# Kernel optimization log

Measured on AMD Instinct MI355X. Metric: run time of the kernel, lower is better.

Reference implementation:

```python
import jax, jax.numpy as jnp
import numpy as np

POS_MARGIN = 0.1
NEG_MARGIN = 1.4
LOG_SCALE = 24.0
MAX_POINTS = 256

N_FULL = 50000
M_C = 2048
N_C = 2048
D_FEAT = 256
K_CORR = 4096
N_BACK = 30000


def setup_inputs() -> dict:
    key = jax.random.key(0)
    ks = jax.random.split(key, 12)
    ref_feats = jax.random.normal(ks[4], (M_C, D_FEAT), jnp.float32)
    src_feats = jax.random.normal(ks[5], (N_C, D_FEAT), jnp.float32)
    # features are assumed L2-normalized (pairwise_distance(..., normalized=True))
    ref_feats = ref_feats / jnp.linalg.norm(ref_feats, axis=-1, keepdims=True)
    src_feats = src_feats / jnp.linalg.norm(src_feats, axis=-1, keepdims=True)
    return {
        "ref_points": jax.random.normal(ks[0], (N_FULL, 3), jnp.float32),
        "src_points": jax.random.normal(ks[1], (N_FULL, 3), jnp.float32),
        "ref_points_c": jax.random.normal(ks[2], (M_C, 3), jnp.float32),
        "src_points_c": jax.random.normal(ks[3], (N_C, 3), jnp.float32),
        "ref_feats_c": ref_feats,
        "src_feats_c": src_feats,
        "gt_node_corr_indices": jax.random.randint(ks[6], (K_CORR, 2), 0, M_C, dtype=jnp.int64) if jax.config.jax_enable_x64 else jax.random.randint(ks[6], (K_CORR, 2), 0, M_C, dtype=jnp.int32),
        "gt_node_corr_overlaps": jax.random.uniform(ks[7], (K_CORR,), jnp.float32),
        "corr_sp_mask": jax.random.uniform(ks[8], (M_C + N_C,), jnp.float32),
        "ref_back_indices": jax.random.randint(ks[9], (N_BACK,), 0, N_FULL, dtype=jnp.int32),
        "src_back_indices": jax.random.randint(ks[10], (N_BACK,), 0, N_FULL, dtype=jnp.int32),
    }


def _nn_indices(full_points, corr_points):
    # argmin over squared euclidean distance == argmin over cdist(p=2)
    d = (jnp.sum(corr_points ** 2, axis=1)[:, None]
         + jnp.sum(full_points ** 2, axis=1)[None, :]
         - 2.0 * corr_points @ full_points.T)  # [k, N]
    return jnp.argmin(d, axis=1)


def _forward(ref_points, src_points, ref_points_c, src_points_c,
             ref_feats_c, src_feats_c, gt_node_corr_overlaps, corr_sp_mask,
             gt_node_corr_indices, ref_back_indices, src_back_indices):
    m = ref_feats_c.shape[0]
    n = src_feats_c.shape[0]

    idx_ref = _nn_indices(ref_points, ref_points_c)  # [m]
    idx_src = _nn_indices(src_points, src_points_c)  # [n]

    # mask_ref[i] True iff idx_ref[i] appears in ref_back_indices (set intersection semantics)
    mask_ref = jnp.any(idx_ref[:, None] == ref_back_indices[None, :], axis=1)
    mask_src = jnp.any(idx_src[:, None] == src_back_indices[None, :], axis=1)

    xi = gt_node_corr_indices[:, 0]
    yi = gt_node_corr_indices[:, 1]
    corr_gt = jnp.zeros((m, n), dtype=bool).at[xi, yi].set(True)
    corr_overlap = jnp.zeros((m, n), jnp.float32).at[xi, yi].set(gt_node_corr_overlaps)

    corr_gt = corr_gt & (mask_ref[:, None] & mask_src[None, :])
    gt_mask = jnp.concatenate([mask_ref, mask_src]).astype(jnp.float32)  # [m+n]

    # cap number of positives at MAX_POINTS by overlap score
    count = jnp.sum(corr_gt)
    score = jnp.where(corr_gt, corr_overlap, -1.0).reshape(-1)
    topv, topi = jax.lax.top_k(score, MAX_POINTS)
    capped = jnp.zeros((m * n,), dtype=bool).at[topi].set(topv > -0.5).reshape(m, n)
    corr_gt = jnp.where(count > MAX_POINTS, capped, corr_gt)

    var_mask = 1.0 - corr_sp_mask  # [m+n]

    # NLLLaplace
    feat_sq = jnp.maximum(2.0 - 2.0 * (ref_feats_c @ src_feats_c.T), 0.0)
    feat_dists = jnp.sqrt(feat_sq)  # [m, n]
    laplace_mask = var_mask[:m][:, None] * var_mask[m:m + n][None, :]
    feat_dists = jnp.exp(0.5 * laplace_mask) * feat_dists

    not_pos = (~corr_gt).astype(jnp.float32)
    not_neg = corr_gt.astype(jnp.float32)
    pos_w = jax.lax.stop_gradient(
        jnp.maximum(feat_dists - 100000.0 * not_pos - POS_MARGIN, 0.0))
    neg_w = jax.lax.stop_gradient(
        jnp.maximum(NEG_MARGIN - (feat_dists + 100000.0 * not_neg), 0.0))

    lp = LOG_SCALE * (feat_dists - POS_MARGIN) * pos_w
    ln = LOG_SCALE * (NEG_MARGIN - feat_dists) * neg_w
    loss_row = jax.nn.softplus(jax.nn.logsumexp(lp, axis=-1) + jax.nn.logsumexp(ln, axis=-1)) / LOG_SCALE
    loss_col = jax.nn.softplus(jax.nn.logsumexp(lp, axis=-2) + jax.nn.logsumexp(ln, axis=-2)) / LOG_SCALE
    loss1 = (jnp.mean(loss_row) + jnp.mean(loss_col)) / 2.0
    loss2 = jnp.mean(jnp.abs(var_mask - gt_mask))
    loss = loss1 + loss2
    return loss, loss1, loss2


def reference(ref_points, src_points, ref_points_c, src_points_c,
              ref_feats_c, src_feats_c, gt_node_corr_indices,
              gt_node_corr_overlaps, corr_sp_mask,
              ref_back_indices, src_back_indices):
    return _forward(ref_points, src_points, ref_points_c, src_points_c,
                    ref_feats_c, src_feats_c, gt_node_corr_overlaps, corr_sp_mask,
                    gt_node_corr_indices, ref_back_indices, src_back_indices)
```

## Files before the change

### kernel.cpp

```cpp
#include <hip/hip_runtime.h>
#include <math.h>

using u8  = unsigned char;
using u32 = unsigned int;
using u64 = unsigned long long;

typedef short short8 __attribute__((ext_vector_type(8)));
typedef float f32x4  __attribute__((ext_vector_type(4)));
typedef float f32x2  __attribute__((ext_vector_type(2)));

#define MC 2048
#define NC 2048
#define DF 256
#define NFULL 50000
#define NBACK 30000
#define KCORR 4096
#define MAXPTS 256
#define NN_CHUNK 196
#define BM_WORDS_I 1568

constexpr size_t OFF_ROWP = 0;
constexpr size_t OFF_COLP = (size_t)2 * 1024 * 1024;
constexpr size_t OFF_GTB  = (size_t)3 * 1024 * 1024;
constexpr size_t OFF_NN   = OFF_GTB + (size_t)512 * 1024;
constexpr size_t OFF_CAND = OFF_NN + 4096 * 8;
constexpr size_t OFF_ACC  = OFF_CAND + 4096 * 8;
constexpr size_t OFF_CNT  = OFF_ACC + 256;
constexpr size_t OFF_BM   = OFF_CNT + 256;
constexpr size_t OFF_KMAX = (size_t)4 * 1024 * 1024;


__device__ __forceinline__ u32 mask_of(const u64* nn, const u32* bm, int idx, int side) {
    u32 j = (u32)(nn[idx] & 0xFFFFFFFFull);
    return (bm[side * BM_WORDS_I + (j >> 5)] >> (j & 31)) & 1u;
}

__device__ __forceinline__ void circle_terms(float d, bool g, float& lp, float& ln) {
    if (g) { float a = d - 0.1f; lp = a > 0.f ? 24.f*a*a : 0.f; ln = 0.f; }
    else   { float b = 1.4f - d; ln = b > 0.f ? 24.f*b*b : 0.f; lp = 0.f; }
}

__device__ __forceinline__ float softplus_(float x) {
    return fmaxf(x, 0.f) + log1pf(expf(-fabsf(x)));
}

__device__ __forceinline__ void lse_merge(float& M, float& S, float M2, float S2) {
    float nm = fmaxf(M, M2);
    S = S * expf(M - nm) + S2 * expf(M2 - nm);
    M = nm;
}

__device__ __forceinline__ void block_barrier(u32* counter, u32 target, u32* s_tic) {
    __threadfence();
    __syncthreads();
    if (threadIdx.x == 0) {
        *s_tic = atomicAdd(counter, 1u);
        while (__hip_atomic_load(counter, __ATOMIC_ACQUIRE, __HIP_MEMORY_SCOPE_AGENT) < target) {}
    }
    __syncthreads();
}

__global__ __launch_bounds__(256) void k_init(uint4* __restrict__ gtb4, u64* __restrict__ nn,
                                              float* __restrict__ acc, u32* __restrict__ cnt,
                                              u32* __restrict__ bm, uint4* __restrict__ kmax4) {
    int e = blockIdx.x * 256 + threadIdx.x;
    #pragma unroll
    for (int u = 0; u < 4; ++u)
        kmax4[e + u * 262144] = make_uint4(0u, 0u, 0u, 0u);
    if (e < 32768) gtb4[e] = make_uint4(0u, 0u, 0u, 0u);
    if (e < 4096) nn[e] = ~0ull;
    if (e < 2 * BM_WORDS_I) bm[e] = 0u;
    if (e < 8) acc[e] = 0.f;
    if (e < 8) cnt[e] = 0u;
}

__global__ __launch_bounds__(256) void k_nn(
        const float* __restrict__ fr, const float* __restrict__ fs,
        const float* __restrict__ cr, const float* __restrict__ cs,
        const int* __restrict__ rbi, const int* __restrict__ sbi,
        u32* __restrict__ bm, u64* __restrict__ nn) {
    const int side = blockIdx.y;
    const float* full = side ? fs : fr;
    const float* corr = side ? cs : cr;
    const int ib = blockIdx.x & 3, ch = blockIdx.x >> 2;
    const int t = threadIdx.x;

    int gb = side * 1024 + blockIdx.x;
    if (gb < 235) {
        int e = gb * 256 + t;
        if (e < 2 * NBACK) {
            int s2 = e < NBACK ? 0 : 1;
            int v = s2 ? sbi[e - NBACK] : rbi[e];
            atomicOr(&bm[s2 * BM_WORDS_I + (v >> 5)], 1u << (v & 31));
        }
    }

    __shared__ float4 sx4[49], sy4[49], sz4[49], sw4[49];
    const int j0 = ch * NN_CHUNK;
    if (t < 49) {
        int b4 = j0 + t * 4;
        float xx[4], yy[4], zz[4], ww[4];
        #pragma unroll
        for (int u = 0; u < 4; ++u) {
            int j = b4 + u;
            if (j < NFULL) {
                float x = full[j*3], y = full[j*3+1], z = full[j*3+2];
                xx[u] = x; yy[u] = y; zz[u] = z;
                ww[u] = fmaf(x, x, fmaf(y, y, z*z));
            } else {
                xx[u] = 0.f; yy[u] = 0.f; zz[u] = 0.f; ww[u] = 3.0e38f;
            }
        }
        sx4[t] = make_float4(xx[0], xx[1], xx[2], xx[3]);
        sy4[t] = make_float4(yy[0], yy[1], yy[2], yy[3]);
        sz4[t] = make_float4(zz[0], zz[1], zz[2], zz[3]);
        sw4[t] = make_float4(ww[0], ww[1], ww[2], ww[3]);
    }

    float ax[2], ay[2], az[2], bd[2];
    int bg[2];
    #pragma unroll
    for (int q = 0; q < 2; ++q) {
        int i = ib * 512 + q * 256 + t;
        float cx = corr[i*3], cy = corr[i*3+1], cz = corr[i*3+2];
        ax[q] = -2.f*cx; ay[q] = -2.f*cy; az[q] = -2.f*cz;
        bd[q] = 3.4e38f; bg[q] = 0;
    }
    __syncthreads();

    #pragma unroll 2
    for (int g = 0; g < 49; ++g) {
        float4 X = sx4[g], Y = sy4[g], Z = sz4[g], W = sw4[g];
        f32x2 xlo = {X.x, X.y}, xhi = {X.z, X.w};
        f32x2 ylo = {Y.x, Y.y}, yhi = {Y.z, Y.w};
        f32x2 zlo = {Z.x, Z.y}, zhi = {Z.z, Z.w};
        f32x2 wlo = {W.x, W.y}, whi = {W.z, W.w};
        #pragma unroll
        for (int q = 0; q < 2; ++q) {
            f32x2 aq = {ax[q], ax[q]}, bq = {ay[q], ay[q]}, cq2 = {az[q], az[q]};
            f32x2 dlo = __builtin_elementwise_fma(aq, xlo,
                          __builtin_elementwise_fma(bq, ylo,
                            __builtin_elementwise_fma(cq2, zlo, wlo)));
            f32x2 dhi = __builtin_elementwise_fma(aq, xhi,
                          __builtin_elementwise_fma(bq, yhi,
                            __builtin_elementwise_fma(cq2, zhi, whi)));
            f32x2 m2 = __builtin_elementwise_min(dlo, dhi);
            float gm = fminf(m2.x, m2.y);
            bool win = gm < bd[q];
            bd[q] = fminf(bd[q], gm);
            bg[q] = win ? g : bg[q];
        }
    }

    #pragma unroll
    for (int q = 0; q < 2; ++q) {
        int gsel = bg[q];
        float4 X = sx4[gsel], Y = sy4[gsel], Z = sz4[gsel], W = sw4[gsel];
        f32x2 xlo = {X.x, X.y}, xhi = {X.z, X.w};
        f32x2 ylo = {Y.x, Y.y}, yhi = {Y.z, Y.w};
        f32x2 zlo = {Z.x, Z.y}, zhi = {Z.z, Z.w};
        f32x2 wlo = {W.x, W.y}, whi = {W.z, W.w};
        f32x2 aq = {ax[q], ax[q]}, bq = {ay[q], ay[q]}, cq2 = {az[q], az[q]};
        f32x2 dlo = __builtin_elementwise_fma(aq, xlo,
                      __builtin_elementwise_fma(bq, ylo,
                        __builtin_elementwise_fma(cq2, zlo, wlo)));
        f32x2 dhi = __builtin_elementwise_fma(aq, xhi,
                      __builtin_elementwise_fma(bq, yhi,
                        __builtin_elementwise_fma(cq2, zhi, whi)));
        float dv[4] = {dlo.x, dlo.y, dhi.x, dhi.y};
        u32 bj = (u32)(j0 + gsel * 4);
        bool found = false;
        #pragma unroll
        for (int u = 0; u < 4; ++u) {
            if (!found && dv[u] == bd[q]) { bj = (u32)(j0 + gsel*4 + u); found = true; }
        }
        int i = ib * 512 + q * 256 + t;
        float cn = 0.25f * fmaf(ax[q], ax[q], fmaf(ay[q], ay[q], az[q]*az[q]));
        float bf = bd[q] + cn;
        u32 db = __float_as_uint(bf);
        db = (db & 0x80000000u) ? ~db : (db | 0x80000000u);
        atomicMin(&nn[side * 2048 + i], ((u64)db << 32) | bj);
    }
}

__global__ __launch_bounds__(256) void k_msc(
        const u64* __restrict__ nn, const u32* __restrict__ bm,
        const float* __restrict__ spm, const int* __restrict__ gti,
        const float* __restrict__ gtv,
        u32* __restrict__ gtb, u32* __restrict__ kmax, u64* __restrict__ cand,
        u32* __restrict__ cnt, float* __restrict__ acc) {
    const int b = blockIdx.x, t = threadIdx.x;
    __shared__ u64 keys[4096];
    __shared__ u32 s_tic;
    __shared__ float red2[4];

    const int e = b * 128 + t;
    float c = 0.f;
    u32 cell = 0, masked = 0;
    if (t < 128) {
        c = fabsf((1.f - spm[e]) - (float)mask_of(nn, bm, e, e >> 11));
        int xi = gti[2*e], yi = gti[2*e+1];
        cell = (u32)(xi * 2048 + yi);
        masked = mask_of(nn, bm, xi, 0) & mask_of(nn, bm, 2048 + yi, 1);
        if (masked) atomicOr(&gtb[xi * 64 + (yi >> 5)], 1u << (yi & 31));
        atomicMax(&kmax[cell], (u32)e + 1u);
    }
    for (int o = 32; o; o >>= 1) c += __shfl_xor(c, o);
    if ((t & 63) == 0) red2[t >> 6] = c;
    __syncthreads();
    if (t == 0) atomicAdd(&acc[2], red2[0] + red2[1] + red2[2] + red2[3]);

    block_barrier(&cnt[2], 32u, &s_tic);

    if (t < 128) {
        u32 wk = __hip_atomic_load(&kmax[cell], __ATOMIC_RELAXED, __HIP_MEMORY_SCOPE_AGENT);
        if (masked && wk == (u32)e + 1u) {
            u32 vb = __float_as_uint(gtv[e]);
            u32 idx = atomicAdd(&cnt[0], 1u);
            cand[idx] = ((u64)vb << 22) | (u32)(0x3FFFFF - cell);
        }
    }
    block_barrier(&cnt[3], 32u, &s_tic);

    if (b < 16) {
        const int n = (int)__hip_atomic_load(&cnt[0], __ATOMIC_RELAXED, __HIP_MEMORY_SCOPE_AGENT);
        if (n > MAXPTS && b * 256 < n) {
            for (int e2 = t; e2 < n; e2 += 256)
                keys[e2] = __hip_atomic_load(&cand[e2], __ATOMIC_RELAXED, __HIP_MEMORY_SCOPE_AGENT);
            __syncthreads();
            int c2 = b * 256 + t;
            if (c2 < n) {
                u64 me = keys[c2];
                int rank = 0;
                #pragma unroll 4
                for (int j = 0; j < n; ++j) rank += (keys[j] > me);
                if (rank >= MAXPTS) {
                    u32 cl = 0x3FFFFFu - (u32)(me & 0x3FFFFFull);
                    int row = cl >> 11, col = cl & 2047;
                    atomicAnd(&gtb[row * 64 + (col >> 5)], ~(1u << (col & 31)));
                }
            }
        }
    }
}

__global__ __launch_bounds__(256) void k_gemm(
        const float* __restrict__ A, const float* __restrict__ B,
        const float* __restrict__ spm, const u32* __restrict__ gtb,
        float4* __restrict__ rowp, float4* __restrict__ colp) {
    __shared__ __align__(16) short As[16384];
    __shared__ __align__(16) short Bs[8192];
    __shared__ u32 gtw[256];
    const int t = threadIdx.x;
    const int l = t & 63, wid = t >> 6;
    const int wm = wid >> 1, wn = wid & 1;
    const int i0 = blockIdx.y * 128, j0 = blockIdx.x * 64;

    gtw[t] = gtb[(size_t)(i0 + (t >> 1)) * 64 + (j0 >> 5) + (t & 1)];

    f32x4 acc[4][2] = {};

    for (int ks = 0; ks < 2; ++ks) {
        __syncthreads();
        #pragma unroll
        for (int it = 0; it < 12; ++it) {
            int sl = it * 256 + t;
            int c = sl & 63, q = c >> 4, r15 = c & 15;
            const float* src;
            short* dst;
            int kf;
            if (it < 8) {
                int frag = sl >> 6;
                kf = frag & 3;
                int row = (frag >> 2) * 16 + r15;
                src = A + (size_t)(i0 + row) * 256;
                dst = &As[sl * 8];
            } else {
                int sl2 = sl - 2048;
                int frag = sl2 >> 6;
                kf = frag & 3;
                int row = (frag >> 2) * 16 + r15;
                src = B + (size_t)(j0 + row) * 256;
                dst = &Bs[sl2 * 8];
            }
            int col = ks * 128 + kf * 32 + q * 8;
            float4 v0 = *(const float4*)(src + col);
            float4 v1 = *(const float4*)(src + col + 4);
            u32 w0 = __builtin_amdgcn_perm(__float_as_uint(v0.y), __float_as_uint(v0.x), 0x07060302u);
            u32 w1 = __builtin_amdgcn_perm(__float_as_uint(v0.w), __float_as_uint(v0.z), 0x07060302u);
            u32 w2 = __builtin_amdgcn_perm(__float_as_uint(v1.y), __float_as_uint(v1.x), 0x07060302u);
            u32 w3 = __builtin_amdgcn_perm(__float_as_uint(v1.w), __float_as_uint(v1.z), 0x07060302u);
            *(uint4*)dst = make_uint4(w0, w1, w2, w3);
        }
        __syncthreads();

        #pragma unroll
        for (int kf = 0; kf < 4; ++kf) {
            short8 a[4], b[2];
            #pragma unroll
            for (int mi = 0; mi < 4; ++mi)
                a[mi] = *(const short8*)&As[(((wm*4 + mi)*4 + kf) << 9) + l*8];
            #pragma unroll
            for (int ni = 0; ni < 2; ++ni)
                b[ni] = *(const short8*)&Bs[(((wn*2 + ni)*4 + kf) << 9) + l*8];
            #pragma unroll
            for (int mi = 0; mi < 4; ++mi)
                #pragma unroll
                for (int ni = 0; ni < 2; ++ni)
                    acc[mi][ni] = __builtin_amdgcn_mfma_f32_16x16x32_bf16(
                        a[mi], b[ni], acc[mi][ni], 0, 0, 0);
        }
    }

    const int cq = l >> 4, cr = l & 15;
    const int rows0 = i0 + wm * 64, cols0 = j0 + wn * 32;

    float vmj[2];
    #pragma unroll
    for (int ni = 0; ni < 2; ++ni) vmj[ni] = 1.f - spm[2048 + cols0 + ni*16 + cr];
    float vmi[4][4];
    #pragma unroll
    for (int mi = 0; mi < 4; ++mi)
        #pragma unroll
        for (int rr = 0; rr < 4; ++rr)
            vmi[mi][rr] = 1.f - spm[rows0 + mi*16 + cq*4 + rr];

    u32 gmask = 0;
    #pragma unroll
    for (int mi = 0; mi < 4; ++mi)
        #pragma unroll
        for (int rr = 0; rr < 4; ++rr) {
            u32 w = gtw[(wm*64 + mi*16 + cq*4 + rr) * 2 + wn];
            #pragma unroll
            for (int ni = 0; ni < 2; ++ni)
                if ((w >> (ni*16 + cr)) & 1u) gmask |= 1u << (mi*8 + ni*4 + rr);
        }
    #pragma unroll
    for (int mi = 0; mi < 4; ++mi)
        #pragma unroll
        for (int ni = 0; ni < 2; ++ni)
            #pragma unroll
            for (int rr = 0; rr < 4; ++rr) {
                float s  = acc[mi][ni][rr];
                float fs = fmaxf(2.f - 2.f*s, 0.f);
                acc[mi][ni][rr] = sqrtf(fs) * expf(0.5f * vmi[mi][rr] * vmj[ni]);
            }

    const int jt2 = blockIdx.x * 2 + wn;
    const int it2 = blockIdx.y * 2 + wm;

    #pragma unroll
    for (int mi = 0; mi < 4; ++mi)
        #pragma unroll
        for (int rr = 0; rr < 4; ++rr) {
            float lp0, ln0, lp1, ln1;
            circle_terms(acc[mi][0][rr], (gmask >> (mi*8 + rr)) & 1, lp0, ln0);
            circle_terms(acc[mi][1][rr], (gmask >> (mi*8 + 4 + rr)) & 1, lp1, ln1);
            float mp = fmaxf(lp0, lp1), mn = fmaxf(ln0, ln1);
            #pragma unroll
            for (int o = 1; o < 16; o <<= 1) {
                mp = fmaxf(mp, __shfl_xor(mp, o));
                mn = fmaxf(mn, __shfl_xor(mn, o));
            }
            float sp = expf(lp0 - mp) + expf(lp1 - mp);
            float sn = expf(ln0 - mn) + expf(ln1 - mn);
            #pragma unroll
            for (int o = 1; o < 16; o <<= 1) {
                sp += __shfl_xor(sp, o);
                sn += __shfl_xor(sn, o);
            }
            if (cr == mi*4 + rr) {
                int row = rows0 + mi*16 + cq*4 + rr;
                rowp[(size_t)jt2 * 2048 + row] = make_float4(mp, sp, mn, sn);
            }
        }

    #pragma unroll
    for (int ni = 0; ni < 2; ++ni) {
        float lp[16], ln[16];
        #pragma unroll
        for (int mi = 0; mi < 4; ++mi)
            #pragma unroll
            for (int rr = 0; rr < 4; ++rr)
                circle_terms(acc[mi][ni][rr], (gmask >> (mi*8 + ni*4 + rr)) & 1,
                             lp[mi*4+rr], ln[mi*4+rr]);
        float mp = lp[0], mn = ln[0];
        #pragma unroll
        for (int e = 1; e < 16; ++e) { mp = fmaxf(mp, lp[e]); mn = fmaxf(mn, ln[e]); }
        #pragma unroll
        for (int o = 16; o < 64; o <<= 1) {
            mp = fmaxf(mp, __shfl_xor(mp, o));
            mn = fmaxf(mn, __shfl_xor(mn, o));
        }
        float sp = 0.f, sn = 0.f;
        #pragma unroll
        for (int e = 0; e < 16; ++e) { sp += expf(lp[e] - mp); sn += expf(ln[e] - mn); }
        #pragma unroll
        for (int o = 16; o < 64; o <<= 1) {
            sp += __shfl_xor(sp, o);
            sn += __shfl_xor(sn, o);
        }
        if (cq == 0) {
            int col = cols0 + ni*16 + cr;
            colp[(size_t)it2 * 2048 + col] = make_float4(mp, sp, mn, sn);
        }
    }
}

__global__ __launch_bounds__(256) void k_merge(const float4* __restrict__ rowp,
                                               const float4* __restrict__ colp,
                                               float* __restrict__ acc,
                                               u32* __restrict__ cnt,
                                               float* __restrict__ out) {
    const int t = threadIdx.x;
    const int b = blockIdx.x;
    const int sub = t & 3;
    float Mp = -1e30f, Sp = 0.f, Mn = -1e30f, Sn = 0.f;

    if (b < 32) {
        int row = (b * 256 + t) >> 2;
        int base = sub * 16;
        #pragma unroll
        for (int j = 0; j < 16; j += 8) {
            float4 pb[8];
            #pragma unroll
            for (int u = 0; u < 8; ++u)
                pb[u] = rowp[(size_t)(base + j + u) * 2048 + row];
            #pragma unroll
            for (int u = 0; u < 8; ++u) {
                lse_merge(Mp, Sp, pb[u].x, pb[u].y);
                lse_merge(Mn, Sn, pb[u].z, pb[u].w);
            }
        }
    } else {
        int col = ((b - 32) * 256 + t) >> 2;
        int base = sub * 8;
        float4 pb[8];
        #pragma unroll
        for (int u = 0; u < 8; ++u)
            pb[u] = colp[(size_t)(base + u) * 2048 + col];
        #pragma unroll
        for (int u = 0; u < 8; ++u) {
            lse_merge(Mp, Sp, pb[u].x, pb[u].y);
            lse_merge(Mn, Sn, pb[u].z, pb[u].w);
        }
    }

    #pragma unroll
    for (int o = 1; o < 4; o <<= 1) {
        float M2 = __shfl_xor(Mp, o), S2 = __shfl_xor(Sp, o);
        lse_merge(Mp, Sp, M2, S2);
        M2 = __shfl_xor(Mn, o); S2 = __shfl_xor(Sn, o);
        lse_merge(Mn, Sn, M2, S2);
    }

    float lv = 0.f;
    if (sub == 0) {
        float x = (Mp + logf(Sp)) + (Mn + logf(Sn));
        lv = softplus_(x) * (1.f / 24.f);
    }
    for (int o = 32; o; o >>= 1) lv += __shfl_xor(lv, o);
    __shared__ float wsum[4];
    __shared__ u32 tic;
    if ((t & 63) == 0) wsum[t >> 6] = lv;
    __syncthreads();
    if (t == 0) {
        atomicAdd(&acc[b < 32 ? 0 : 1], wsum[0] + wsum[1] + wsum[2] + wsum[3]);
        __threadfence();
        tic = atomicAdd(&cnt[1], 1u);
    }
    __syncthreads();
    if (t == 0 && tic == 63u) {
        __threadfence();
        float a0 = atomicAdd(&acc[0], 0.f);
        float a1 = atomicAdd(&acc[1], 0.f);
        float a2 = atomicAdd(&acc[2], 0.f);
        float l1 = (a0 + a1) * (0.5f / 2048.f);
        float l2 = a2 * (1.f / 4096.f);
        out[0] = l1 + l2; out[1] = l1; out[2] = l2;
    }
}

extern "C" void kernel_launch(void* const* d_in, const int* in_sizes, int n_in,
                              void* d_out, int out_size, void* d_ws, size_t ws_size,
                              hipStream_t stream) {
    (void)in_sizes; (void)n_in; (void)out_size; (void)ws_size;
    const float* ref_points = (const float*)d_in[0];
    const float* src_points = (const float*)d_in[1];
    const float* ref_c      = (const float*)d_in[2];
    const float* src_c      = (const float*)d_in[3];
    const float* ref_f      = (const float*)d_in[4];
    const float* src_f      = (const float*)d_in[5];
    const int*   gti        = (const int*)d_in[6];
    const float* gtv        = (const float*)d_in[7];
    const float* spm        = (const float*)d_in[8];
    const int*   rbi        = (const int*)d_in[9];
    const int*   sbi        = (const int*)d_in[10];

    char* ws = (char*)d_ws;
    float4* rowp = (float4*)(ws + OFF_ROWP);
    float4* colp = (float4*)(ws + OFF_COLP);
    u32*   gtb  = (u32*)  (ws + OFF_GTB);
    u64*   nn   = (u64*)  (ws + OFF_NN);
    u64*   cand = (u64*)  (ws + OFF_CAND);
    float* acc  = (float*)(ws + OFF_ACC);
    u32*   cnt  = (u32*)  (ws + OFF_CNT);
    u32*   bm   = (u32*)  (ws + OFF_BM);
    u32*   kmax = (u32*)  (ws + OFF_KMAX);

    k_init <<<1024, 256, 0, stream>>>((uint4*)gtb, nn, acc, cnt, bm, (uint4*)kmax);
    k_nn   <<<dim3(1024, 2), 256, 0, stream>>>(ref_points, src_points, ref_c, src_c,
                                               rbi, sbi, bm, nn);
    k_msc  <<<32, 256, 0, stream>>>(nn, bm, spm, gti, gtv, gtb, kmax, cand, cnt, acc);
    k_gemm <<<dim3(32, 16), 256, 0, stream>>>(ref_f, src_f, spm, gtb, rowp, colp);
    k_merge<<<64, 256, 0, stream>>>(rowp, colp, acc, cnt, (float*)d_out);
}
```

Baseline: 101.2 us.

## Replace grid spin barriers with separate kernels and sparse kmax clearing

The k_msc kernel used two software grid-wide spin barriers. It is now split into three kernels: mark, scatter candidates and top-k rank, so kernel boundaries provide the ordering instead. k_init no longer zeroes the full 16MB kmax table. It clears only the 4096 cells indexed by gt correspondences, which cuts a large memory write. The cost is two extra kernel launches and a per-element mcell buffer.

```diff
diff --git a/kernel.cpp b/kernel.cpp
--- a/kernel.cpp
+++ b/kernel.cpp
@@ -24,7 +24,8 @@
 constexpr size_t OFF_GTB  = (size_t)3 * 1024 * 1024;
 constexpr size_t OFF_NN   = OFF_GTB + (size_t)512 * 1024;
 constexpr size_t OFF_CAND = OFF_NN + 4096 * 8;
-constexpr size_t OFF_ACC  = OFF_CAND + 4096 * 8;
+constexpr size_t OFF_MC   = OFF_CAND + 4096 * 8;
+constexpr size_t OFF_ACC  = OFF_MC + 4096 * 4;
 constexpr size_t OFF_CNT  = OFF_ACC + 256;
 constexpr size_t OFF_BM   = OFF_CNT + 256;
 constexpr size_t OFF_KMAX = (size_t)4 * 1024 * 1024;
@@ -50,25 +51,17 @@
     M = nm;
 }
 
-__device__ __forceinline__ void block_barrier(u32* counter, u32 target, u32* s_tic) {
-    __threadfence();
-    __syncthreads();
-    if (threadIdx.x == 0) {
-        *s_tic = atomicAdd(counter, 1u);
-        while (__hip_atomic_load(counter, __ATOMIC_ACQUIRE, __HIP_MEMORY_SCOPE_AGENT) < target) {}
-    }
-    __syncthreads();
-}
-
 __global__ __launch_bounds__(256) void k_init(uint4* __restrict__ gtb4, u64* __restrict__ nn,
                                               float* __restrict__ acc, u32* __restrict__ cnt,
-                                              u32* __restrict__ bm, uint4* __restrict__ kmax4) {
+                                              u32* __restrict__ bm, u32* __restrict__ kmax,
+                                              const int* __restrict__ gti) {
     int e = blockIdx.x * 256 + threadIdx.x;
-    #pragma unroll
-    for (int u = 0; u < 4; ++u)
-        kmax4[e + u * 262144] = make_uint4(0u, 0u, 0u, 0u);
-    if (e < 32768) gtb4[e] = make_uint4(0u, 0u, 0u, 0u);
-    if (e < 4096) nn[e] = ~0ull;
+    gtb4[e] = make_uint4(0u, 0u, 0u, 0u);
+    if (e < 4096) {
+        nn[e] = ~0ull;
+        int xi = gti[2*e], yi = gti[2*e+1];
+        kmax[xi * 2048 + yi] = 0u;
+    }
     if (e < 2 * BM_WORDS_I) bm[e] = 0u;
     if (e < 8) acc[e] = 0.f;
     if (e < 8) cnt[e] = 0u;
@@ -186,61 +179,59 @@
 __global__ __launch_bounds__(256) void k_msc(
         const u64* __restrict__ nn, const u32* __restrict__ bm,
         const float* __restrict__ spm, const int* __restrict__ gti,
-        const float* __restrict__ gtv,
-        u32* __restrict__ gtb, u32* __restrict__ kmax, u64* __restrict__ cand,
-        u32* __restrict__ cnt, float* __restrict__ acc) {
+        u32* __restrict__ gtb, u32* __restrict__ kmax, u32* __restrict__ mcell,
+        float* __restrict__ acc) {
     const int b = blockIdx.x, t = threadIdx.x;
-    __shared__ u64 keys[4096];
-    __shared__ u32 s_tic;
+    const int e = b * 256 + t;
     __shared__ float red2[4];
 
-    const int e = b * 128 + t;
-    float c = 0.f;
-    u32 cell = 0, masked = 0;
-    if (t < 128) {
-        c = fabsf((1.f - spm[e]) - (float)mask_of(nn, bm, e, e >> 11));
-        int xi = gti[2*e], yi = gti[2*e+1];
-        cell = (u32)(xi * 2048 + yi);
-        masked = mask_of(nn, bm, xi, 0) & mask_of(nn, bm, 2048 + yi, 1);
-        if (masked) atomicOr(&gtb[xi * 64 + (yi >> 5)], 1u << (yi & 31));
-        atomicMax(&kmax[cell], (u32)e + 1u);
-    }
+    float c = fabsf((1.f - spm[e]) - (float)mask_of(nn, bm, e, e >> 11));
+    int xi = gti[2*e], yi = gti[2*e+1];
+    u32 cell = (u32)(xi * 2048 + yi);
+    u32 masked = mask_of(nn, bm, xi, 0) & mask_of(nn, bm, 2048 + yi, 1);
+    if (masked) atomicOr(&gtb[xi * 64 + (yi >> 5)], 1u << (yi & 31));
+    atomicMax(&kmax[cell], (u32)e + 1u);
+    mcell[e] = cell | (masked << 31);
+
     for (int o = 32; o; o >>= 1) c += __shfl_xor(c, o);
     if ((t & 63) == 0) red2[t >> 6] = c;
     __syncthreads();
     if (t == 0) atomicAdd(&acc[2], red2[0] + red2[1] + red2[2] + red2[3]);
-
-    block_barrier(&cnt[2], 32u, &s_tic);
-
-    if (t < 128) {
-        u32 wk = __hip_atomic_load(&kmax[cell], __ATOMIC_RELAXED, __HIP_MEMORY_SCOPE_AGENT);
-        if (masked && wk == (u32)e + 1u) {
-            u32 vb = __float_as_uint(gtv[e]);
-            u32 idx = atomicAdd(&cnt[0], 1u);
-            cand[idx] = ((u64)vb << 22) | (u32)(0x3FFFFF - cell);
-        }
-    }
-    block_barrier(&cnt[3], 32u, &s_tic);
-
-    if (b < 16) {
-        const int n = (int)__hip_atomic_load(&cnt[0], __ATOMIC_RELAXED, __HIP_MEMORY_SCOPE_AGENT);
-        if (n > MAXPTS && b * 256 < n) {
-            for (int e2 = t; e2 < n; e2 += 256)
-                keys[e2] = __hip_atomic_load(&cand[e2], __ATOMIC_RELAXED, __HIP_MEMORY_SCOPE_AGENT);
-            __syncthreads();
-            int c2 = b * 256 + t;
-            if (c2 < n) {
-                u64 me = keys[c2];
-                int rank = 0;
-                #pragma unroll 4
-                for (int j = 0; j < n; ++j) rank += (keys[j] > me);
-                if (rank >= MAXPTS) {
-                    u32 cl = 0x3FFFFFu - (u32)(me & 0x3FFFFFull);
-                    int row = cl >> 11, col = cl & 2047;
-                    atomicAnd(&gtb[row * 64 + (col >> 5)], ~(1u << (col & 31)));
-                }
-            }
-        }
+}
+
+__global__ __launch_bounds__(256) void k_scat2(
+        const u32* __restrict__ kmax, const u32* __restrict__ mcell,
+        const float* __restrict__ gtv, u64* __restrict__ cand, u32* __restrict__ cnt) {
+    const int e = blockIdx.x * 256 + threadIdx.x;
+    u32 mc = mcell[e];
+    if (!(mc >> 31)) return;
+    u32 cell = mc & 0x3FFFFFu;
+    if (kmax[cell] != (u32)e + 1u) return;
+    u32 vb = __float_as_uint(gtv[e]);
+    u32 idx = atomicAdd(&cnt[0], 1u);
+    cand[idx] = ((u64)vb << 22) | (u32)(0x3FFFFF - cell);
+}
+
+__global__ __launch_bounds__(256) void k_top(const u64* __restrict__ cand,
+                                             const u32* __restrict__ cnt,
+                                             u32* __restrict__ gtb) {
+    const int n = (int)cnt[0];
+    if (n <= MAXPTS) return;
+    if (blockIdx.x * 256 >= n) return;
+    __shared__ u64 keys[4096];
+    const int t = threadIdx.x;
+    for (int e = t; e < n; e += 256) keys[e] = cand[e];
+    __syncthreads();
+    int c = blockIdx.x * 256 + t;
+    if (c >= n) return;
+    u64 me = keys[c];
+    int rank = 0;
+    #pragma unroll 4
+    for (int j = 0; j < n; ++j) rank += (keys[j] > me);
+    if (rank >= MAXPTS) {
+        u32 cell = 0x3FFFFFu - (u32)(me & 0x3FFFFFull);
+        int row = cell >> 11, col = cell & 2047;
+        atomicAnd(&gtb[row * 64 + (col >> 5)], ~(1u << (col & 31)));
     }
 }
 
@@ -503,15 +494,18 @@
     u32*   gtb  = (u32*)  (ws + OFF_GTB);
     u64*   nn   = (u64*)  (ws + OFF_NN);
     u64*   cand = (u64*)  (ws + OFF_CAND);
+    u32*   mcell= (u32*)  (ws + OFF_MC);
     float* acc  = (float*)(ws + OFF_ACC);
     u32*   cnt  = (u32*)  (ws + OFF_CNT);
     u32*   bm   = (u32*)  (ws + OFF_BM);
     u32*   kmax = (u32*)  (ws + OFF_KMAX);
 
-    k_init <<<1024, 256, 0, stream>>>((uint4*)gtb, nn, acc, cnt, bm, (uint4*)kmax);
+    k_init <<<128, 256, 0, stream>>>((uint4*)gtb, nn, acc, cnt, bm, kmax, gti);
     k_nn   <<<dim3(1024, 2), 256, 0, stream>>>(ref_points, src_points, ref_c, src_c,
                                                rbi, sbi, bm, nn);
-    k_msc  <<<32, 256, 0, stream>>>(nn, bm, spm, gti, gtv, gtb, kmax, cand, cnt, acc);
+    k_msc  <<<16, 256, 0, stream>>>(nn, bm, spm, gti, gtb, kmax, mcell, acc);
+    k_scat2<<<16, 256, 0, stream>>>(kmax, mcell, gtv, cand, cnt);
+    k_top  <<<16, 256, 0, stream>>>(cand, cnt, gtb);
     k_gemm <<<dim3(32, 16), 256, 0, stream>>>(ref_f, src_f, spm, gtb, rowp, colp);
     k_merge<<<64, 256, 0, stream>>>(rowp, colp, acc, cnt, (float*)d_out);
 }
```

Measured after the change: 95.57 us. 5.6% less time.
